# Kernel optimization log

Measured on AMD Instinct MI355X. Metric: run time of the kernel, lower is better.

The kernel has to match this reference:

```python
import jax, jax.numpy as jnp
import numpy as np

B, T, D, H = 1024, 256, 128, 64

def setup_inputs() -> dict:
    key = jax.random.key(0)
    ks = jax.random.split(key, 9)
    s = 1.0 / np.sqrt(H)  # PyTorch LSTM init scale
    x = jax.random.normal(ks[0], (B, T, D), dtype=jnp.float32)
    W_ih = jax.random.uniform(ks[1], (4 * H, D), dtype=jnp.float32, minval=-s, maxval=s)
    W_hh = jax.random.uniform(ks[2], (4 * H, H), dtype=jnp.float32, minval=-s, maxval=s)
    b_ih = jax.random.uniform(ks[3], (4 * H,), dtype=jnp.float32, minval=-s, maxval=s)
    b_hh = jax.random.uniform(ks[4], (4 * H,), dtype=jnp.float32, minval=-s, maxval=s)
    W1 = jax.random.uniform(ks[5], (32, H), dtype=jnp.float32, minval=-s, maxval=s)
    b1 = jax.random.uniform(ks[6], (32,), dtype=jnp.float32, minval=-s, maxval=s)
    W2 = jax.random.uniform(ks[7], (1, 32), dtype=jnp.float32, minval=-0.18, maxval=0.18)
    b2 = jax.random.uniform(ks[8], (1,), dtype=jnp.float32, minval=-0.18, maxval=0.18)
    return {"x": x, "W_ih": W_ih, "W_hh": W_hh, "b_ih": b_ih, "b_hh": b_hh,
            "W1": W1, "b1": b1, "W2": W2, "b2": b2}

def reference(x, W_ih, W_hh, b_ih, b_hh, W1, b1, W2, b2):
    b = b_ih + b_hh
    # Precompute input-to-hidden projections for all timesteps: [B,T,4H]
    x_proj = jnp.einsum('btd,gd->btg', x, W_ih) + b

    def step(carry, xp_t):
        h, c = carry
        gates = xp_t + h @ W_hh.T  # [B,4H]
        i, f, g, o = jnp.split(gates, 4, axis=-1)  # PyTorch gate order
        i = jax.nn.sigmoid(i)
        f = jax.nn.sigmoid(f)
        g = jnp.tanh(g)
        o = jax.nn.sigmoid(o)
        c = f * c + i * g
        h = o * jnp.tanh(c)
        return (h, c), None

    h0 = jnp.zeros((x.shape[0], H), dtype=x.dtype)
    c0 = jnp.zeros((x.shape[0], H), dtype=x.dtype)
    (h, _), _ = jax.lax.scan(step, (h0, c0), jnp.swapaxes(x_proj, 0, 1))  # scan over T

    y = jax.nn.relu(h @ W1.T + b1)  # [B,32]
    y = jax.nn.sigmoid(y @ W2.T + b2)  # [B,1]
    return y.reshape(-1)
```

## Files before the change

kernel.cpp:

```cpp
#include <hip/hip_runtime.h>
#include <math.h>

constexpr int B_ = 1024;
constexpr int T_ = 256;
constexpr int D_ = 128;
constexpr int H_ = 64;

typedef short  v8s __attribute__((ext_vector_type(8)));
typedef float  v4f __attribute__((ext_vector_type(4)));

__device__ __forceinline__ float sigmoidf_(float x) {
    return 1.0f / (1.0f + __expf(-x));
}
__device__ __forceinline__ float tanhf_(float x) {
    return fmaf(2.0f, 1.0f / (1.0f + __expf(-2.0f * x)), -1.0f);
}
__device__ __forceinline__ unsigned short f2bf(float f) {
    unsigned u = __float_as_uint(f);
    u = (u + 0x7fffu + ((u >> 16) & 1u)) >> 16;
    return (unsigned short)u;
}
__device__ __forceinline__ v8s pack8(float4 a, float4 b) {
    v8s r;
    r[0] = (short)f2bf(a.x); r[1] = (short)f2bf(a.y);
    r[2] = (short)f2bf(a.z); r[3] = (short)f2bf(a.w);
    r[4] = (short)f2bf(b.x); r[5] = (short)f2bf(b.y);
    r[6] = (short)f2bf(b.z); r[7] = (short)f2bf(b.w);
    return r;
}

__global__ __launch_bounds__(256, 1)
void lstm_mono_kernel(const float* __restrict__ x,
                      const float* __restrict__ W_ih,
                      const float* __restrict__ W_hh,
                      const float* __restrict__ b_ih,
                      const float* __restrict__ b_hh,
                      const float* __restrict__ W1,
                      const float* __restrict__ b1,
                      const float* __restrict__ W2,
                      const float* __restrict__ b2,
                      float* __restrict__ out)
{
    const int bb   = blockIdx.x;
    const int tid  = threadIdx.x;
    const int wv   = tid >> 6;
    const int lane = tid & 63;
    const int q    = lane >> 4;
    const int ml   = lane & 15;

    __shared__ __align__(16) unsigned short xbuf[2][8][16][136];
    __shared__ __align__(16) unsigned short hbf[2][16][72];
    __shared__ __align__(16) float hf[16][68];
    __shared__ __align__(16) float ys[16][36];

    v8s wih[4][4];
    v8s whh[4][2];
    v4f bias[4];
    #pragma unroll
    for (int cls = 0; cls < 4; ++cls) {
        const int gr = (cls * 4 + wv) * 16 + ml;
        #pragma unroll
        for (int ks = 0; ks < 4; ++ks) {
            const float* p = W_ih + (size_t)gr * D_ + ks * 32 + q * 8;
            wih[cls][ks] = pack8(((const float4*)p)[0], ((const float4*)p)[1]);
        }
        #pragma unroll
        for (int ks = 0; ks < 2; ++ks) {
            const float* p = W_hh + (size_t)gr * H_ + ks * 32 + q * 8;
            whh[cls][ks] = pack8(((const float4*)p)[0], ((const float4*)p)[1]);
        }
        #pragma unroll
        for (int r = 0; r < 4; ++r) {
            const int g2 = (cls * 4 + wv) * 16 + q * 4 + r;
            bias[cls][r] = b_ih[g2] + b_hh[g2];
        }
    }

    for (int i = tid; i < 1152; i += 256) ((unsigned*)hbf)[i] = 0u;

    const float* __restrict__ xb = x + (size_t)(bb * 16) * T_ * D_;
    const int stl = tid >> 5;
    const int sc4 = tid & 31;

    #pragma unroll
    for (int bt = 0; bt < 16; ++bt) {
        float4 v = ((const float4*)(xb + ((size_t)bt * T_ + stl) * D_))[sc4];
        short4 s;
        s.x = (short)f2bf(v.x); s.y = (short)f2bf(v.y);
        s.z = (short)f2bf(v.z); s.w = (short)f2bf(v.w);
        *(short4*)&xbuf[0][stl][bt][sc4 * 4] = s;
    }
    __syncthreads();

    float cst[4]   = {0.f, 0.f, 0.f, 0.f};
    float hlast[4] = {0.f, 0.f, 0.f, 0.f};

    v4f xacc[4];
    #pragma unroll
    for (int cls = 0; cls < 4; ++cls) xacc[cls] = bias[cls];
    #pragma unroll
    for (int ks = 0; ks < 4; ++ks) {
        v8s bf = *(const v8s*)&xbuf[0][0][ml][ks * 32 + q * 8];
        #pragma unroll
        for (int cls = 0; cls < 4; ++cls)
            xacc[cls] = __builtin_amdgcn_mfma_f32_16x16x32_bf16(
                wih[cls][ks], bf, xacc[cls], 0, 0, 0);
    }

    for (int w32 = 0; w32 < 32; ++w32) {
        const int  wp    = w32 & 1;
        const bool stage = (w32 < 31);
        float4 sA[4], sB[4];

        #pragma unroll
        for (int tl = 0; tl < 8; ++tl) {
            if (stage) {
                if (tl == 0) {
                    #pragma unroll
                    for (int j = 0; j < 4; ++j)
                        sA[j] = ((const float4*)(xb + ((size_t)(j) * T_
                                 + (w32 + 1) * 8 + stl) * D_))[sc4];
                } else if (tl == 1) {
                    #pragma unroll
                    for (int j = 0; j < 4; ++j)
                        sB[j] = ((const float4*)(xb + ((size_t)(4 + j) * T_
                                 + (w32 + 1) * 8 + stl) * D_))[sc4];
                } else if (tl == 2) {
                    #pragma unroll
                    for (int j = 0; j < 4; ++j)
                        sA[j] = ((const float4*)(xb + ((size_t)(8 + j) * T_
                                 + (w32 + 1) * 8 + stl) * D_))[sc4];
                } else if (tl == 3) {
                    #pragma unroll
                    for (int j = 0; j < 4; ++j)
                        sB[j] = ((const float4*)(xb + ((size_t)(12 + j) * T_
                                 + (w32 + 1) * 8 + stl) * D_))[sc4];
                }
            }

            v8s h0 = *(const v8s*)&hbf[tl & 1][ml][q * 8];
            v8s h1 = *(const v8s*)&hbf[tl & 1][ml][32 + q * 8];
            v4f acc[4];
            #pragma unroll
            for (int cls = 0; cls < 4; ++cls) {
                acc[cls] = __builtin_amdgcn_mfma_f32_16x16x32_bf16(
                    whh[cls][0], h0, xacc[cls], 0, 0, 0);
                acc[cls] = __builtin_amdgcn_mfma_f32_16x16x32_bf16(
                    whh[cls][1], h1, acc[cls], 0, 0, 0);
            }

            {
                const int nslot = (tl == 7) ? 1 - wp : wp;
                const int tln   = (tl + 1) & 7;
                v4f xn[4];
                #pragma unroll
                for (int cls = 0; cls < 4; ++cls) xn[cls] = bias[cls];
                #pragma unroll
                for (int ks = 0; ks < 4; ++ks) {
                    v8s bf = *(const v8s*)&xbuf[nslot][tln][ml][ks * 32 + q * 8];
                    #pragma unroll
                    for (int cls = 0; cls < 4; ++cls)
                        xn[cls] = __builtin_amdgcn_mfma_f32_16x16x32_bf16(
                            wih[cls][ks], bf, xn[cls], 0, 0, 0);
                }
                #pragma unroll
                for (int cls = 0; cls < 4; ++cls) xacc[cls] = xn[cls];
            }

            if (stage) {
                if (tl == 1 || tl == 3) {
                    const int c0 = (tl == 1) ? 0 : 8;
                    #pragma unroll
                    for (int j = 0; j < 4; ++j) {
                        float4 v = sA[j];
                        short4 s;
                        s.x = (short)f2bf(v.x); s.y = (short)f2bf(v.y);
                        s.z = (short)f2bf(v.z); s.w = (short)f2bf(v.w);
                        *(short4*)&xbuf[1 - wp][stl][c0 + j][sc4 * 4] = s;
                    }
                } else if (tl == 2 || tl == 4) {
                    const int c0 = (tl == 2) ? 4 : 12;
                    #pragma unroll
                    for (int j = 0; j < 4; ++j) {
                        float4 v = sB[j];
                        short4 s;
                        s.x = (short)f2bf(v.x); s.y = (short)f2bf(v.y);
                        s.z = (short)f2bf(v.z); s.w = (short)f2bf(v.w);
                        *(short4*)&xbuf[1 - wp][stl][c0 + j][sc4 * 4] = s;
                    }
                }
            }

            #pragma unroll
            for (int r = 0; r < 4; ++r) {
                float gi = sigmoidf_(acc[0][r]);
                float gf = sigmoidf_(acc[1][r]);
                float gg = tanhf_(acc[2][r]);
                float go = sigmoidf_(acc[3][r]);
                cst[r]   = fmaf(gf, cst[r], gi * gg);
                hlast[r] = go * tanhf_(cst[r]);
            }

            {
                ushort4 hp;
                hp.x = f2bf(hlast[0]); hp.y = f2bf(hlast[1]);
                hp.z = f2bf(hlast[2]); hp.w = f2bf(hlast[3]);
                *(ushort4*)&hbf[1 - (tl & 1)][ml][wv * 16 + q * 4] = hp;
            }

            __syncthreads();
        }
    }

    {
        float4 hv;
        hv.x = hlast[0]; hv.y = hlast[1]; hv.z = hlast[2]; hv.w = hlast[3];
        *(float4*)&hf[ml][wv * 16 + q * 4] = hv;
    }
    __syncthreads();
    {
        const int bloc = tid & 15, jj = tid >> 4;
        #pragma unroll
        for (int j2 = 0; j2 < 2; ++j2) {
            const int j = jj + j2 * 16;
            float acc = b1[j];
            const float4* w1r = (const float4*)(W1 + (size_t)j * H_);
            #pragma unroll
            for (int k4 = 0; k4 < 16; ++k4) {
                float4 h4 = *(const float4*)&hf[bloc][k4 * 4];
                float4 w4 = w1r[k4];
                acc = fmaf(w4.x, h4.x, acc); acc = fmaf(w4.y, h4.y, acc);
                acc = fmaf(w4.z, h4.z, acc); acc = fmaf(w4.w, h4.w, acc);
            }
            ys[bloc][j] = fmaxf(acc, 0.0f);
        }
    }
    __syncthreads();
    if (tid < 16) {
        float a = b2[0];
        #pragma unroll
        for (int j = 0; j < 32; ++j) a = fmaf(W2[j], ys[tid][j], a);
        out[bb * 16 + tid] = sigmoidf_(a);
    }
}

extern "C" void kernel_launch(void* const* d_in, const int* in_sizes, int n_in,
                              void* d_out, int out_size, void* d_ws, size_t ws_size,
                              hipStream_t stream) {
    const float* x    = (const float*)d_in[0];
    const float* W_ih = (const float*)d_in[1];
    const float* W_hh = (const float*)d_in[2];
    const float* b_ih = (const float*)d_in[3];
    const float* b_hh = (const float*)d_in[4];
    const float* W1   = (const float*)d_in[5];
    const float* b1   = (const float*)d_in[6];
    const float* W2   = (const float*)d_in[7];
    const float* b2   = (const float*)d_in[8];
    float* out = (float*)d_out;

    lstm_mono_kernel<<<dim3(B_ / 16), dim3(256), 0, stream>>>(
        x, W_ih, W_hh, b_ih, b_hh, W1, b1, W2, b2, out);
}
```

Before: 453.2 us.

## Split LSTM block into producer and consumer warps with LDS counters

Each block is split into four producer wavefronts and four recurrent consumer wavefronts. The producers compute the input projections straight from global memory and stage them as bf16 in double-buffered LDS. The consumers run the h·W_hh recurrence and sync among themselves with LDS atomic counters and spin-waits instead of __syncthreads. Each block now handles 8 batch rows instead of 16, so there are twice as many blocks and two blocks per CU. This is meant to take the input projection off the serial recurrence path and raise parallelism. The cost is wasted half-tiles in the MFMA (rows 8-15 are padding), an extra bf16 rounding of the projection, and spin-wait overhead.

```diff
diff --git a/kernel.cpp b/kernel.cpp
--- a/kernel.cpp
+++ b/kernel.cpp
@@ -5,6 +5,8 @@
 constexpr int T_ = 256;
 constexpr int D_ = 128;
 constexpr int H_ = 64;
+constexpr int BPB_ = 8;
+constexpr int NBLK_ = B_ / BPB_;
 
 typedef short  v8s __attribute__((ext_vector_type(8)));
 typedef float  v4f __attribute__((ext_vector_type(4)));
@@ -29,218 +31,215 @@
     return r;
 }
 
-__global__ __launch_bounds__(256, 1)
-void lstm_mono_kernel(const float* __restrict__ x,
-                      const float* __restrict__ W_ih,
-                      const float* __restrict__ W_hh,
-                      const float* __restrict__ b_ih,
-                      const float* __restrict__ b_hh,
-                      const float* __restrict__ W1,
-                      const float* __restrict__ b1,
-                      const float* __restrict__ W2,
-                      const float* __restrict__ b2,
-                      float* __restrict__ out)
+__global__ __launch_bounds__(512, 2)
+void lstm_pc_kernel(const float* __restrict__ x,
+                    const float* __restrict__ W_ih,
+                    const float* __restrict__ W_hh,
+                    const float* __restrict__ b_ih,
+                    const float* __restrict__ b_hh,
+                    const float* __restrict__ W1,
+                    const float* __restrict__ b1,
+                    const float* __restrict__ W2,
+                    const float* __restrict__ b2,
+                    float* __restrict__ out)
 {
-    const int bb   = blockIdx.x;
     const int tid  = threadIdx.x;
     const int wv   = tid >> 6;
     const int lane = tid & 63;
     const int q    = lane >> 4;
     const int ml   = lane & 15;
-
-    __shared__ __align__(16) unsigned short xbuf[2][8][16][136];
+    const int mlc  = ml & 7;
+
+    __shared__ __align__(16) ushort4 xpbuf[2][8][BPB_][66];
     __shared__ __align__(16) unsigned short hbf[2][16][72];
     __shared__ __align__(16) float hf[16][68];
-    __shared__ __align__(16) float ys[16][36];
-
-    v8s wih[4][4];
-    v8s whh[4][2];
-    v4f bias[4];
-    #pragma unroll
-    for (int cls = 0; cls < 4; ++cls) {
-        const int gr = (cls * 4 + wv) * 16 + ml;
-        #pragma unroll
-        for (int ks = 0; ks < 4; ++ks) {
-            const float* p = W_ih + (size_t)gr * D_ + ks * 32 + q * 8;
-            wih[cls][ks] = pack8(((const float4*)p)[0], ((const float4*)p)[1]);
-        }
-        #pragma unroll
-        for (int ks = 0; ks < 2; ++ks) {
-            const float* p = W_hh + (size_t)gr * H_ + ks * 32 + q * 8;
-            whh[cls][ks] = pack8(((const float4*)p)[0], ((const float4*)p)[1]);
-        }
-        #pragma unroll
-        for (int r = 0; r < 4; ++r) {
-            const int g2 = (cls * 4 + wv) * 16 + q * 4 + r;
-            bias[cls][r] = b_ih[g2] + b_hh[g2];
-        }
-    }
-
-    for (int i = tid; i < 1152; i += 256) ((unsigned*)hbf)[i] = 0u;
-
-    const float* __restrict__ xb = x + (size_t)(bb * 16) * T_ * D_;
-    const int stl = tid >> 5;
-    const int sc4 = tid & 31;
-
-    #pragma unroll
-    for (int bt = 0; bt < 16; ++bt) {
-        float4 v = ((const float4*)(xb + ((size_t)bt * T_ + stl) * D_))[sc4];
-        short4 s;
-        s.x = (short)f2bf(v.x); s.y = (short)f2bf(v.y);
-        s.z = (short)f2bf(v.z); s.w = (short)f2bf(v.w);
-        *(short4*)&xbuf[0][stl][bt][sc4 * 4] = s;
-    }
+    __shared__ __align__(16) float ys[BPB_][36];
+    __shared__ unsigned pcnt[2];
+    __shared__ unsigned ccnt[2];
+    __shared__ unsigned hcnt;
+
+    if (tid == 0) { pcnt[0] = 0; pcnt[1] = 0; ccnt[0] = 0; ccnt[1] = 0; hcnt = 0; }
+    for (int i = tid; i < 2 * 16 * 72 / 2; i += 512) ((unsigned*)hbf)[i] = 0u;
     __syncthreads();
 
-    float cst[4]   = {0.f, 0.f, 0.f, 0.f};
-    float hlast[4] = {0.f, 0.f, 0.f, 0.f};
-
-    v4f xacc[4];
-    #pragma unroll
-    for (int cls = 0; cls < 4; ++cls) xacc[cls] = bias[cls];
-    #pragma unroll
-    for (int ks = 0; ks < 4; ++ks) {
-        v8s bf = *(const v8s*)&xbuf[0][0][ml][ks * 32 + q * 8];
-        #pragma unroll
-        for (int cls = 0; cls < 4; ++cls)
-            xacc[cls] = __builtin_amdgcn_mfma_f32_16x16x32_bf16(
-                wih[cls][ks], bf, xacc[cls], 0, 0, 0);
-    }
-
-    for (int w32 = 0; w32 < 32; ++w32) {
-        const int  wp    = w32 & 1;
-        const bool stage = (w32 < 31);
-        float4 sA[4], sB[4];
-
-        #pragma unroll
-        for (int tl = 0; tl < 8; ++tl) {
-            if (stage) {
-                if (tl == 0) {
-                    #pragma unroll
-                    for (int j = 0; j < 4; ++j)
-                        sA[j] = ((const float4*)(xb + ((size_t)(j) * T_
-                                 + (w32 + 1) * 8 + stl) * D_))[sc4];
-                } else if (tl == 1) {
-                    #pragma unroll
-                    for (int j = 0; j < 4; ++j)
-                        sB[j] = ((const float4*)(xb + ((size_t)(4 + j) * T_
-                                 + (w32 + 1) * 8 + stl) * D_))[sc4];
-                } else if (tl == 2) {
-                    #pragma unroll
-                    for (int j = 0; j < 4; ++j)
-                        sA[j] = ((const float4*)(xb + ((size_t)(8 + j) * T_
-                                 + (w32 + 1) * 8 + stl) * D_))[sc4];
-                } else if (tl == 3) {
-                    #pragma unroll
-                    for (int j = 0; j < 4; ++j)
-                        sB[j] = ((const float4*)(xb + ((size_t)(12 + j) * T_
-                                 + (w32 + 1) * 8 + stl) * D_))[sc4];
-                }
-            }
-
-            v8s h0 = *(const v8s*)&hbf[tl & 1][ml][q * 8];
-            v8s h1 = *(const v8s*)&hbf[tl & 1][ml][32 + q * 8];
-            v4f acc[4];
+    const float* __restrict__ xb = x + (size_t)(blockIdx.x * BPB_) * T_ * D_;
+
+    if (wv >= 4) {
+        const int pw = wv - 4;
+        v8s wih[4][4];
+        v4f bias[4];
+        #pragma unroll
+        for (int cls = 0; cls < 4; ++cls) {
+            const int gr = (cls * 4 + pw) * 16 + ml;
             #pragma unroll
-            for (int cls = 0; cls < 4; ++cls) {
-                acc[cls] = __builtin_amdgcn_mfma_f32_16x16x32_bf16(
-                    whh[cls][0], h0, xacc[cls], 0, 0, 0);
-                acc[cls] = __builtin_amdgcn_mfma_f32_16x16x32_bf16(
-                    whh[cls][1], h1, acc[cls], 0, 0, 0);
-            }
-
-            {
-                const int nslot = (tl == 7) ? 1 - wp : wp;
-                const int tln   = (tl + 1) & 7;
-                v4f xn[4];
-                #pragma unroll
-                for (int cls = 0; cls < 4; ++cls) xn[cls] = bias[cls];
+            for (int ks = 0; ks < 4; ++ks) {
+                const float* p = W_ih + (size_t)gr * D_ + ks * 32 + q * 8;
+                wih[cls][ks] = pack8(((const float4*)p)[0], ((const float4*)p)[1]);
+            }
+            #pragma unroll
+            for (int r = 0; r < 4; ++r) {
+                const int g2 = (cls * 4 + pw) * 16 + q * 4 + r;
+                bias[cls][r] = b_ih[g2] + b_hh[g2];
+            }
+        }
+
+        for (int w = 0; w < 32; ++w) {
+            const int s = w & 1, e = w >> 1;
+            if (e >= 1) {
+                const unsigned tgt = 4u * (unsigned)e;
+                while (*(volatile const unsigned*)&ccnt[s] < tgt)
+                    __builtin_amdgcn_s_sleep(1);
+                __threadfence_block();
+            }
+            #pragma unroll 2
+            for (int tl = 0; tl < 8; ++tl) {
+                const int t = w * 8 + tl;
+                v4f acc[4];
+                #pragma unroll
+                for (int cls = 0; cls < 4; ++cls) acc[cls] = bias[cls];
                 #pragma unroll
                 for (int ks = 0; ks < 4; ++ks) {
-                    v8s bf = *(const v8s*)&xbuf[nslot][tln][ml][ks * 32 + q * 8];
+                    v8s bfr;
+                    if (ml < BPB_) {
+                        const float* p = xb + ((size_t)ml * T_ + t) * D_
+                                            + ks * 32 + q * 8;
+                        bfr = pack8(((const float4*)p)[0], ((const float4*)p)[1]);
+                    } else {
+                        bfr = (v8s)(short)0;
+                    }
                     #pragma unroll
                     for (int cls = 0; cls < 4; ++cls)
-                        xn[cls] = __builtin_amdgcn_mfma_f32_16x16x32_bf16(
-                            wih[cls][ks], bf, xn[cls], 0, 0, 0);
-                }
-                #pragma unroll
-                for (int cls = 0; cls < 4; ++cls) xacc[cls] = xn[cls];
-            }
-
-            if (stage) {
-                if (tl == 1 || tl == 3) {
-                    const int c0 = (tl == 1) ? 0 : 8;
+                        acc[cls] = __builtin_amdgcn_mfma_f32_16x16x32_bf16(
+                            wih[cls][ks], bfr, acc[cls], 0, 0, 0);
+                }
+                if (ml < BPB_) {
                     #pragma unroll
-                    for (int j = 0; j < 4; ++j) {
-                        float4 v = sA[j];
-                        short4 s;
-                        s.x = (short)f2bf(v.x); s.y = (short)f2bf(v.y);
-                        s.z = (short)f2bf(v.z); s.w = (short)f2bf(v.w);
-                        *(short4*)&xbuf[1 - wp][stl][c0 + j][sc4 * 4] = s;
+                    for (int r = 0; r < 4; ++r) {
+                        ushort4 p;
+                        p.x = f2bf(acc[0][r]);
+                        p.y = f2bf(acc[1][r]);
+                        p.z = f2bf(acc[2][r]);
+                        p.w = f2bf(acc[3][r]);
+                        xpbuf[s][tl][ml][pw * 16 + q * 4 + r] = p;
                     }
-                } else if (tl == 2 || tl == 4) {
-                    const int c0 = (tl == 2) ? 4 : 12;
-                    #pragma unroll
-                    for (int j = 0; j < 4; ++j) {
-                        float4 v = sB[j];
-                        short4 s;
-                        s.x = (short)f2bf(v.x); s.y = (short)f2bf(v.y);
-                        s.z = (short)f2bf(v.z); s.w = (short)f2bf(v.w);
-                        *(short4*)&xbuf[1 - wp][stl][c0 + j][sc4 * 4] = s;
-                    }
-                }
-            }
-
+                }
+            }
+            __threadfence_block();
+            if (lane == 0) atomicAdd(&pcnt[s], 1u);
+        }
+    } else {
+        v8s whh[4][2];
+        #pragma unroll
+        for (int cls = 0; cls < 4; ++cls) {
+            const int gr = (cls * 4 + wv) * 16 + ml;
             #pragma unroll
-            for (int r = 0; r < 4; ++r) {
-                float gi = sigmoidf_(acc[0][r]);
-                float gf = sigmoidf_(acc[1][r]);
-                float gg = tanhf_(acc[2][r]);
-                float go = sigmoidf_(acc[3][r]);
-                cst[r]   = fmaf(gf, cst[r], gi * gg);
-                hlast[r] = go * tanhf_(cst[r]);
-            }
-
+            for (int ks = 0; ks < 2; ++ks) {
+                const float* p = W_hh + (size_t)gr * H_ + ks * 32 + q * 8;
+                whh[cls][ks] = pack8(((const float4*)p)[0], ((const float4*)p)[1]);
+            }
+        }
+
+        float cst[4]   = {0.f, 0.f, 0.f, 0.f};
+        float hlast[4] = {0.f, 0.f, 0.f, 0.f};
+
+        for (int w = 0; w < 32; ++w) {
+            const int s = w & 1, e = w >> 1;
             {
+                const unsigned tgt = 4u * (unsigned)(e + 1);
+                while (*(volatile const unsigned*)&pcnt[s] < tgt)
+                    __builtin_amdgcn_s_sleep(1);
+                __threadfence_block();
+            }
+            uint4 A, Bv;
+            {
+                const uint4* xpp = (const uint4*)&xpbuf[s][0][mlc][wv * 16 + q * 4];
+                A = xpp[0]; Bv = xpp[1];
+            }
+            #pragma unroll 2
+            for (int tl = 0; tl < 8; ++tl) {
+                const int t = w * 8 + tl;
+                v8s h0 = *(const v8s*)&hbf[tl & 1][ml][q * 8];
+                v8s h1 = *(const v8s*)&hbf[tl & 1][ml][32 + q * 8];
+                uint4 An, Bn;
+                if (tl < 7) {
+                    const uint4* xpp =
+                        (const uint4*)&xpbuf[s][tl + 1][mlc][wv * 16 + q * 4];
+                    An = xpp[0]; Bn = xpp[1];
+                }
+                v4f acc[4];
+                acc[0][0] = __uint_as_float(A.x << 16);
+                acc[1][0] = __uint_as_float(A.x & 0xffff0000u);
+                acc[2][0] = __uint_as_float(A.y << 16);
+                acc[3][0] = __uint_as_float(A.y & 0xffff0000u);
+                acc[0][1] = __uint_as_float(A.z << 16);
+                acc[1][1] = __uint_as_float(A.z & 0xffff0000u);
+                acc[2][1] = __uint_as_float(A.w << 16);
+                acc[3][1] = __uint_as_float(A.w & 0xffff0000u);
+                acc[0][2] = __uint_as_float(Bv.x << 16);
+                acc[1][2] = __uint_as_float(Bv.x & 0xffff0000u);
+                acc[2][2] = __uint_as_float(Bv.y << 16);
+                acc[3][2] = __uint_as_float(Bv.y & 0xffff0000u);
+                acc[0][3] = __uint_as_float(Bv.z << 16);
+                acc[1][3] = __uint_as_float(Bv.z & 0xffff0000u);
+                acc[2][3] = __uint_as_float(Bv.w << 16);
+                acc[3][3] = __uint_as_float(Bv.w & 0xffff0000u);
+                #pragma unroll
+                for (int cls = 0; cls < 4; ++cls) {
+                    acc[cls] = __builtin_amdgcn_mfma_f32_16x16x32_bf16(
+                        whh[cls][0], h0, acc[cls], 0, 0, 0);
+                    acc[cls] = __builtin_amdgcn_mfma_f32_16x16x32_bf16(
+                        whh[cls][1], h1, acc[cls], 0, 0, 0);
+                }
+                #pragma unroll
+                for (int r = 0; r < 4; ++r) {
+                    float gi = sigmoidf_(acc[0][r]);
+                    float gf = sigmoidf_(acc[1][r]);
+                    float gg = tanhf_(acc[2][r]);
+                    float go = sigmoidf_(acc[3][r]);
+                    cst[r]   = fmaf(gf, cst[r], gi * gg);
+                    hlast[r] = go * tanhf_(cst[r]);
+                }
                 ushort4 hp;
                 hp.x = f2bf(hlast[0]); hp.y = f2bf(hlast[1]);
                 hp.z = f2bf(hlast[2]); hp.w = f2bf(hlast[3]);
                 *(ushort4*)&hbf[1 - (tl & 1)][ml][wv * 16 + q * 4] = hp;
-            }
-
-            __syncthreads();
-        }
-    }
-
-    {
+                __threadfence_block();
+                if (lane == 0) atomicAdd(&hcnt, 1u);
+                const unsigned tgt = 4u * (unsigned)(t + 1);
+                while (*(volatile const unsigned*)&hcnt < tgt) { }
+                __threadfence_block();
+                A = An; Bv = Bn;
+            }
+            __threadfence_block();
+            if (lane == 0) atomicAdd(&ccnt[s], 1u);
+        }
         float4 hv;
         hv.x = hlast[0]; hv.y = hlast[1]; hv.z = hlast[2]; hv.w = hlast[3];
         *(float4*)&hf[ml][wv * 16 + q * 4] = hv;
     }
+
     __syncthreads();
-    {
-        const int bloc = tid & 15, jj = tid >> 4;
-        #pragma unroll
-        for (int j2 = 0; j2 < 2; ++j2) {
-            const int j = jj + j2 * 16;
-            float acc = b1[j];
-            const float4* w1r = (const float4*)(W1 + (size_t)j * H_);
-            #pragma unroll
-            for (int k4 = 0; k4 < 16; ++k4) {
-                float4 h4 = *(const float4*)&hf[bloc][k4 * 4];
-                float4 w4 = w1r[k4];
-                acc = fmaf(w4.x, h4.x, acc); acc = fmaf(w4.y, h4.y, acc);
-                acc = fmaf(w4.z, h4.z, acc); acc = fmaf(w4.w, h4.w, acc);
-            }
-            ys[bloc][j] = fmaxf(acc, 0.0f);
-        }
+
+    if (tid < 256) {
+        const int bloc = tid & 7;
+        const int j    = tid >> 3;
+        float acc = b1[j];
+        const float4* w1r = (const float4*)(W1 + (size_t)j * H_);
+        #pragma unroll
+        for (int k4 = 0; k4 < 16; ++k4) {
+            float4 h4 = *(const float4*)&hf[bloc][k4 * 4];
+            float4 w4 = w1r[k4];
+            acc = fmaf(w4.x, h4.x, acc); acc = fmaf(w4.y, h4.y, acc);
+            acc = fmaf(w4.z, h4.z, acc); acc = fmaf(w4.w, h4.w, acc);
+        }
+        ys[bloc][j] = fmaxf(acc, 0.0f);
     }
     __syncthreads();
-    if (tid < 16) {
+    if (tid < BPB_) {
         float a = b2[0];
         #pragma unroll
         for (int j = 0; j < 32; ++j) a = fmaf(W2[j], ys[tid][j], a);
-        out[bb * 16 + tid] = sigmoidf_(a);
+        out[blockIdx.x * BPB_ + tid] = sigmoidf_(a);
     }
 }
 
@@ -258,6 +257,6 @@
     const float* b2   = (const float*)d_in[8];
     float* out = (float*)d_out;
 
-    lstm_mono_kernel<<<dim3(B_ / 16), dim3(256), 0, stream>>>(
+    lstm_pc_kernel<<<dim3(NBLK_), dim3(512), 0, stream>>>(
         x, W_ih, W_hh, b_ih, b_hh, W1, b1, W2, b2, out);
 }
```

Result: slower. 770.6 us (+70.1%).
